# Kernel tuning notes

Hardware: AMD Instinct MI355X
Metric: run time of the kernel (lower is better)

Reference implementation:

```python
import jax, jax.numpy as jnp
from jax import lax
import numpy as np

B, CIN, COUT, T, H, W, KH, KW = 8, 256, 256, 16, 28, 28, 3, 3


def setup_inputs() -> dict:
    key = jax.random.key(0)
    k1, k2, k3 = jax.random.split(key, 3)
    x = jax.random.normal(k1, (B, CIN, T, H, W), dtype=jnp.float32)
    alpha = jax.random.uniform(k2, (B, CIN, T, 1, 1), dtype=jnp.float32)
    # base weight, kaiming-uniform-like init, stored as [1,1,c_out,c_in,kh,kw]
    fan_in = CIN * KH * KW
    bound = 1.0 / np.sqrt(fan_in)
    weight = jax.random.uniform(k3, (1, 1, COUT, CIN, KH, KW), dtype=jnp.float32,
                                minval=-bound, maxval=bound)
    return {"x": x, "alpha": alpha, "weight": weight}


def reference(x, alpha, weight):
    # x: [b, c_in, t, h, w]; alpha: [b, c_in, t, 1, 1]; weight: [1,1,c_out,c_in,kh,kw]
    b, c_in, t, h, w = x.shape
    c_out = weight.shape[2]
    w_base = weight[0, 0]  # [c_out, c_in, kh, kw]
    # W_t = alpha_t * W_base scales only input channels (alpha broadcasts over c_out),
    # so (alpha*W) conv x == W conv (alpha*x): modulate input, then one shared conv.
    xm = x * alpha  # [b, c_in, t, h, w]
    xm = jnp.transpose(xm, (0, 2, 1, 3, 4)).reshape(b * t, c_in, h, w)
    y = lax.conv_general_dilated(
        xm, w_base,
        window_strides=(1, 1),
        padding=((1, 1), (1, 1)),
        dimension_numbers=("NCHW", "OIHW", "NCHW"),
    )  # [b*t, c_out, h, w]
    oh, ow = y.shape[-2], y.shape[-1]
    y = y.reshape(b, t, c_out, oh, ow)
    return jnp.transpose(y, (0, 2, 1, 3, 4))  # [b, c_out, t, h, w]
```

## Files before the change

kernel.cpp:

```cpp
#include <hip/hip_runtime.h>
#include <hip/hip_bf16.h>
#include <cstdint>

#define CIN   256
#define COUT  256
#define NB    8
#define NT    16
#define NH    28
#define NW    28
#define HP    30
#define WP    30

#define XM_ELEMS   ((size_t)NB * NT * HP * WP * CIN)
#define XM_BYTES   (XM_ELEMS * 2)

typedef __bf16 bf16x8 __attribute__((ext_vector_type(8)));
typedef float  f32x4  __attribute__((ext_vector_type(4)));

#define AS1 __attribute__((address_space(1)))
#define AS3 __attribute__((address_space(3)))

static __device__ __forceinline__ unsigned short f2bf(float f) {
    __hip_bfloat16 h = __float2bfloat16(f);
    return __builtin_bit_cast(unsigned short, h);
}

__global__ void modulate_kernel(const float* __restrict__ x,
                                const float* __restrict__ alpha,
                                unsigned short* __restrict__ xm) {
    const int ci = threadIdx.x;
    const int blk = blockIdx.x;
    const int hp = blk % 30;
    const int bt = blk / 30;
    unsigned short* row = xm + (size_t)(bt * 900 + hp * 30) * 256;
    if (hp == 0 || hp == 29) {
        #pragma unroll
        for (int wp = 0; wp < 30; ++wp) row[wp * 256 + ci] = 0;
        return;
    }
    const int t = bt & 15, b = bt >> 4;
    const int h = hp - 1;
    const float a = alpha[(b * CIN + ci) * NT + t];
    const float* xrow = x + ((size_t)((b * CIN + ci) * NT + t) * NH + h) * NW;
    row[ci] = 0;
    row[29 * 256 + ci] = 0;
    const float4* xv = (const float4*)xrow;
    #pragma unroll
    for (int q = 0; q < 7; ++q) {
        float4 v = xv[q];
        row[(q * 4 + 1) * 256 + ci] = f2bf(v.x * a);
        row[(q * 4 + 2) * 256 + ci] = f2bf(v.y * a);
        row[(q * 4 + 3) * 256 + ci] = f2bf(v.z * a);
        row[(q * 4 + 4) * 256 + ci] = f2bf(v.w * a);
    }
}

__global__ void repack_w_kernel(const float* __restrict__ w,
                                unsigned short* __restrict__ wB) {
    const int ci = threadIdx.x;
    const int tap = blockIdx.x >> 8;
    const int co  = blockIdx.x & 255;
    wB[((tap * 256 + co) * 256) + ci] = f2bf(w[(co * 256 + ci) * 9 + tap]);
}


#define STAGE_A4(buf, off) do {                                               \
    _Pragma("unroll") for (int c_ = 0; c_ < 4; ++c_)                          \
        __builtin_amdgcn_global_load_lds(                                     \
            (const AS1 void*)(aSrc + (off) + c_ * 16384),                     \
            (AS3 void*)(lds + (buf)*32768 + c_*4096 + wave*512 + lane*8),     \
            16, 0, 0);                                                        \
} while (0)

#define STAGE_B4(buf, off) do {                                               \
    __builtin_amdgcn_global_load_lds((const AS1 void*)(bP0 + (off)),          \
        (AS3 void*)(lds + (buf)*32768 + 16384 + 0*4096 + wave*512 + lane*8), 16, 0, 0); \
    __builtin_amdgcn_global_load_lds((const AS1 void*)(bP1 + (off)),          \
        (AS3 void*)(lds + (buf)*32768 + 16384 + 1*4096 + wave*512 + lane*8), 16, 0, 0); \
    __builtin_amdgcn_global_load_lds((const AS1 void*)(bP2 + (off)),          \
        (AS3 void*)(lds + (buf)*32768 + 16384 + 2*4096 + wave*512 + lane*8), 16, 0, 0); \
    __builtin_amdgcn_global_load_lds((const AS1 void*)(bP3 + (off)),          \
        (AS3 void*)(lds + (buf)*32768 + 16384 + 3*4096 + wave*512 + lane*8), 16, 0, 0); \
} while (0)

#define READ_FA(buf) do {                                                     \
    _Pragma("unroll") for (int m_ = 0; m_ < 4; ++m_)                          \
    _Pragma("unroll") for (int kk_ = 0; kk_ < 2; ++kk_)                       \
        fa[m_][kk_] = *(const bf16x8*)(ldsc + (buf)*65536 +                   \
            (wm*64 + m_*16 + l15)*128 + (frag_sw ^ (kk_<<6)));                \
} while (0)

#define READ_FB4(buf, base) do {                                              \
    _Pragma("unroll") for (int f_ = 0; f_ < 4; ++f_)                          \
    _Pragma("unroll") for (int kk_ = 0; kk_ < 2; ++kk_)                       \
        fb[f_][kk_] = *(const bf16x8*)(ldsc + (buf)*65536 + 32768 +           \
            (wn*112 + ((base)+f_)*16 + l15)*128 + (frag_sw ^ (kk_<<6)));      \
} while (0)

#define READ_FB3(buf, base) do {                                              \
    _Pragma("unroll") for (int f_ = 0; f_ < 3; ++f_)                          \
    _Pragma("unroll") for (int kk_ = 0; kk_ < 2; ++kk_)                       \
        fb[f_][kk_] = *(const bf16x8*)(ldsc + (buf)*65536 + 32768 +           \
            (wn*112 + ((base)+f_)*16 + l15)*128 + (frag_sw ^ (kk_<<6)));      \
} while (0)

#define MFMA_A() do {                                                         \
    _Pragma("unroll") for (int m_ = 0; m_ < 4; ++m_)                          \
    _Pragma("unroll") for (int f_ = 0; f_ < 4; ++f_)                          \
    _Pragma("unroll") for (int kk_ = 0; kk_ < 2; ++kk_)                       \
        acc[m_][f_] = __builtin_amdgcn_mfma_f32_16x16x32_bf16(                \
            fb[f_][kk_], fa[m_][kk_], acc[m_][f_], 0, 0, 0);                  \
} while (0)

#define MFMA_B() do {                                                         \
    _Pragma("unroll") for (int m_ = 0; m_ < 4; ++m_)                          \
    _Pragma("unroll") for (int f_ = 0; f_ < 3; ++f_)                          \
    _Pragma("unroll") for (int kk_ = 0; kk_ < 2; ++kk_)                       \
        acc[m_][4+f_] = __builtin_amdgcn_mfma_f32_16x16x32_bf16(              \
            fb[f_][kk_], fa[m_][kk_], acc[m_][4+f_], 0, 0, 0);                \
} while (0)

#define BAR()   __builtin_amdgcn_s_barrier()
#define LGKM0() asm volatile("s_waitcnt lgkmcnt(0)")
#define VMW(N)  asm volatile("s_waitcnt vmcnt(" #N ")" ::: "memory")
#define PRIO(x) __builtin_amdgcn_s_setprio(x)

#define OFFA(kt) (((kt) >> 2) * 65536 + ((kt) & 3) * 64)
#define OFFB(kt) (((((kt) >> 2) / 3) - 1) * 7680 + ((((kt) >> 2) % 3) - 1) * 256 + ((kt) & 3) * 64)

__global__ __launch_bounds__(512, 2) void conv_gemm_kernel(
    const unsigned short* __restrict__ xm,
    const unsigned short* __restrict__ wB,
    float* __restrict__ out) {
    __shared__ unsigned short lds[65536];

    const int tid  = threadIdx.x;
    const int wave = tid >> 6;
    const int lane = tid & 63;
    const int n0   = blockIdx.x * 224;
    const int wm   = wave >> 1;
    const int wn   = wave & 1;
    const int l15  = lane & 15;

    const int swz8 = 8 * ((lane & 7) ^ (lane >> 3));
    const unsigned short* aSrc = wB + (wave * 8 + (lane >> 3)) * 256 + swz8;

    auto bcent = [&](int rowl) -> const unsigned short* {
        int r = rowl > 223 ? 223 : rowl;
        int n = n0 + r;
        int w_ = n % 28, h_ = (n / 28) % 28, bt = n / 784;
        return xm + (size_t)((bt * 30 + h_ + 1) * 30 + (w_ + 1)) * 256 + swz8;
    };
    const unsigned short* bP0 = bcent(0 * 64 + wave * 8 + (lane >> 3));
    const unsigned short* bP1 = bcent(1 * 64 + wave * 8 + (lane >> 3));
    const unsigned short* bP2 = bcent(2 * 64 + wave * 8 + (lane >> 3));
    const unsigned short* bP3 = bcent(3 * 64 + wave * 8 + (lane >> 3));

    const char* ldsc = (const char*)lds;
    const int frag_sw = ((lane >> 4) * 16) ^ ((lane & 7) << 4);

    f32x4 acc[4][7];
    #pragma unroll
    for (int i = 0; i < 4; ++i)
        #pragma unroll
        for (int j = 0; j < 7; ++j) acc[i][j] = f32x4{0.f,0.f,0.f,0.f};

    bf16x8 fa[4][2], fb[4][2];

    STAGE_A4(0, 0);
    STAGE_B4(0, OFFB(0));
    STAGE_A4(1, OFFA(1));
    VMW(4);
    BAR();

    #pragma unroll 1
    for (int it = 0; it < 17; ++it) {
        const int kt1 = 2 * it + 1;
        const int ka  = 2 * it + 2;
        const int kb  = 2 * it + 3;
        const int offB_k1 = OFFB(kt1);
        const int offA_ka = OFFA(ka);
        const int offB_ka = OFFB(ka);
        const int offA_kb = OFFA(kb);

        READ_FA(0); READ_FB4(0, 0);
        STAGE_B4(1, offB_k1);
        BAR(); LGKM0(); PRIO(1); MFMA_A(); PRIO(0); BAR();
        READ_FB3(0, 4);
        STAGE_A4(0, offA_ka);
        VMW(4);
        BAR(); LGKM0(); PRIO(1); MFMA_B(); PRIO(0); BAR();
        READ_FA(1); READ_FB4(1, 0);
        STAGE_B4(0, offB_ka);
        BAR(); LGKM0(); PRIO(1); MFMA_A(); PRIO(0); BAR();
        READ_FB3(1, 4);
        STAGE_A4(1, offA_kb);
        VMW(4);
        BAR(); LGKM0(); PRIO(1); MFMA_B(); PRIO(0); BAR();
    }

    {
        READ_FA(0); READ_FB4(0, 0);
        STAGE_B4(1, OFFB(35));
        BAR(); LGKM0(); PRIO(1); MFMA_A(); PRIO(0); BAR();
        READ_FB3(0, 4);
        VMW(0);
        BAR(); LGKM0(); PRIO(1); MFMA_B(); PRIO(0); BAR();
        READ_FA(1); READ_FB4(1, 0);
        LGKM0(); PRIO(1); MFMA_A(); PRIO(0);
        READ_FB3(1, 4);
        LGKM0(); PRIO(1); MFMA_B(); PRIO(0);
    }

    #pragma unroll
    for (int f = 0; f < 7; ++f) {
        const int n  = n0 + wn * 112 + f * 16 + ((lane >> 4) << 2);
        const int bt = n / 784;
        const int hw = n - bt * 784;
        const int b = bt >> 4, t = bt & 15;
        float* obase = out + ((size_t)(b * 256) * 16 + t) * 784 + hw;
        #pragma unroll
        for (int m = 0; m < 4; ++m) {
            const int co = wm * 64 + m * 16 + l15;
            *(f32x4*)(obase + (size_t)co * 12544) = acc[m][f];
        }
    }
}

extern "C" void kernel_launch(void* const* d_in, const int* in_sizes, int n_in,
                              void* d_out, int out_size, void* d_ws, size_t ws_size,
                              hipStream_t stream) {
    const float* x      = (const float*)d_in[0];
    const float* alpha  = (const float*)d_in[1];
    const float* weight = (const float*)d_in[2];
    float* out = (float*)d_out;

    unsigned short* xm = (unsigned short*)d_ws;
    unsigned short* wB = (unsigned short*)((char*)d_ws + XM_BYTES);

    modulate_kernel<<<dim3(NB * NT * HP), dim3(256), 0, stream>>>(x, alpha, xm);
    repack_w_kernel<<<dim3(9 * 256), dim3(256), 0, stream>>>(weight, wB);
    conv_gemm_kernel<<<dim3(448), dim3(512), 0, stream>>>(xm, wB, out);
}
```

Baseline: 162.5 us.

## Stage padded input halo once per channel block and reuse across taps

Result: slower. 313.1 us (+92.6%).

```diff
diff --git a/kernel.cpp b/kernel.cpp
--- a/kernel.cpp
+++ b/kernel.cpp
@@ -13,6 +13,7 @@
 
 #define XM_ELEMS   ((size_t)NB * NT * HP * WP * CIN)
 #define XM_BYTES   (XM_ELEMS * 2)
+#define SPAT_MAX   (NB * NT * HP * WP - 1)
 
 typedef __bf16 bf16x8 __attribute__((ext_vector_type(8)));
 typedef float  f32x4  __attribute__((ext_vector_type(4)));
@@ -64,44 +65,47 @@
 }
 
 
-#define STAGE_A4(buf, off) do {                                               \
+#define STAGE_A(abuf, offE) do {                                              \
     _Pragma("unroll") for (int c_ = 0; c_ < 4; ++c_)                          \
         __builtin_amdgcn_global_load_lds(                                     \
-            (const AS1 void*)(aSrc + (off) + c_ * 16384),                     \
-            (AS3 void*)(lds + (buf)*32768 + c_*4096 + wave*512 + lane*8),     \
+            (const AS1 void*)(aSrc + (offE) + c_ * 16384),                    \
+            (AS3 void*)(lds + (abuf)*16384 + c_*4096 + wave*512 + lane*8),    \
             16, 0, 0);                                                        \
 } while (0)
 
-#define STAGE_B4(buf, off) do {                                               \
-    __builtin_amdgcn_global_load_lds((const AS1 void*)(bP0 + (off)),          \
-        (AS3 void*)(lds + (buf)*32768 + 16384 + 0*4096 + wave*512 + lane*8), 16, 0, 0); \
-    __builtin_amdgcn_global_load_lds((const AS1 void*)(bP1 + (off)),          \
-        (AS3 void*)(lds + (buf)*32768 + 16384 + 1*4096 + wave*512 + lane*8), 16, 0, 0); \
-    __builtin_amdgcn_global_load_lds((const AS1 void*)(bP2 + (off)),          \
-        (AS3 void*)(lds + (buf)*32768 + 16384 + 2*4096 + wave*512 + lane*8), 16, 0, 0); \
-    __builtin_amdgcn_global_load_lds((const AS1 void*)(bP3 + (off)),          \
-        (AS3 void*)(lds + (buf)*32768 + 16384 + 3*4096 + wave*512 + lane*8), 16, 0, 0); \
-} while (0)
-
-#define READ_FA(buf) do {                                                     \
+#define STAGE_HALO(hbuf, ci0) do {                                            \
+    _Pragma("unroll") for (int c_ = 0; c_ < 5; ++c_) {                        \
+        int row_ = c_*64 + wave*8 + (lane>>3);                                \
+        int spat_ = haloSpat0 + row_;                                         \
+        spat_ = spat_ > SPAT_MAX ? SPAT_MAX : spat_;                          \
+        __builtin_amdgcn_global_load_lds(                                     \
+            (const AS1 void*)(xm + (size_t)spat_*256 + (ci0) + swz8),         \
+            (AS3 void*)(lds + 32768 + (hbuf)*23040 + (c_*64 + wave*8)*64 + lane*8), \
+            16, 0, 0);                                                        \
+    }                                                                         \
+    {   int rg_ = (wave < 5) ? (320 + wave*8) : ((wave - 5)*8);               \
+        int row_ = rg_ + (lane>>3);                                           \
+        int spat_ = haloSpat0 + row_;                                         \
+        spat_ = spat_ > SPAT_MAX ? SPAT_MAX : spat_;                          \
+        __builtin_amdgcn_global_load_lds(                                     \
+            (const AS1 void*)(xm + (size_t)spat_*256 + (ci0) + swz8),         \
+            (AS3 void*)(lds + 32768 + (hbuf)*23040 + rg_*64 + lane*8),        \
+            16, 0, 0); }                                                      \
+} while (0)
+
+#define READ_FA(abuf) do {                                                    \
     _Pragma("unroll") for (int m_ = 0; m_ < 4; ++m_)                          \
     _Pragma("unroll") for (int kk_ = 0; kk_ < 2; ++kk_)                       \
-        fa[m_][kk_] = *(const bf16x8*)(ldsc + (buf)*65536 +                   \
-            (wm*64 + m_*16 + l15)*128 + (frag_sw ^ (kk_<<6)));                \
-} while (0)
-
-#define READ_FB4(buf, base) do {                                              \
-    _Pragma("unroll") for (int f_ = 0; f_ < 4; ++f_)                          \
-    _Pragma("unroll") for (int kk_ = 0; kk_ < 2; ++kk_)                       \
-        fb[f_][kk_] = *(const bf16x8*)(ldsc + (buf)*65536 + 32768 +           \
-            (wn*112 + ((base)+f_)*16 + l15)*128 + (frag_sw ^ (kk_<<6)));      \
-} while (0)
-
-#define READ_FB3(buf, base) do {                                              \
-    _Pragma("unroll") for (int f_ = 0; f_ < 3; ++f_)                          \
-    _Pragma("unroll") for (int kk_ = 0; kk_ < 2; ++kk_)                       \
-        fb[f_][kk_] = *(const bf16x8*)(ldsc + (buf)*65536 + 32768 +           \
-            (wn*112 + ((base)+f_)*16 + l15)*128 + (frag_sw ^ (kk_<<6)));      \
+        fa[m_][kk_] = *(const bf16x8*)(lds + (abuf)*16384 +                   \
+            (wm*64 + m_*16 + l15)*64 + (kslot ^ (kk_*32)));                   \
+} while (0)
+
+#define READ_FB1(slot, hbuf, f_, TO) do {                                     \
+    const int row_ = localB[f_] + (TO);                                       \
+    const int sw_  = ((lane>>4)*8) ^ ((row_ & 7)*8);                          \
+    _Pragma("unroll") for (int kk_ = 0; kk_ < 2; ++kk_)                       \
+        fb[slot][kk_] = *(const bf16x8*)(lds + 32768 + (hbuf)*23040 +         \
+            row_*64 + (sw_ ^ (kk_*32)));                                      \
 } while (0)
 
 #define MFMA_A() do {                                                         \
@@ -121,18 +125,14 @@
 } while (0)
 
 #define BAR()   __builtin_amdgcn_s_barrier()
-#define LGKM0() asm volatile("s_waitcnt lgkmcnt(0)")
 #define VMW(N)  asm volatile("s_waitcnt vmcnt(" #N ")" ::: "memory")
 #define PRIO(x) __builtin_amdgcn_s_setprio(x)
-
-#define OFFA(kt) (((kt) >> 2) * 65536 + ((kt) & 3) * 64)
-#define OFFB(kt) (((((kt) >> 2) / 3) - 1) * 7680 + ((((kt) >> 2) % 3) - 1) * 256 + ((kt) & 3) * 64)
 
 __global__ __launch_bounds__(512, 2) void conv_gemm_kernel(
     const unsigned short* __restrict__ xm,
     const unsigned short* __restrict__ wB,
     float* __restrict__ out) {
-    __shared__ unsigned short lds[65536];
+    __shared__ unsigned short lds[78848];
 
     const int tid  = threadIdx.x;
     const int wave = tid >> 6;
@@ -141,24 +141,25 @@
     const int wm   = wave >> 1;
     const int wn   = wave & 1;
     const int l15  = lane & 15;
-
-    const int swz8 = 8 * ((lane & 7) ^ (lane >> 3));
+    const int kslot = ((lane >> 4) * 8) ^ ((l15 & 7) * 8);
+
+    const int r0 = blockIdx.x * 8;
+    const int prow_start = r0 + 2 * (r0 / 28);
+    const int haloSpat0  = prow_start * 30;
+
+    int localB[7];
+    #pragma unroll
+    for (int f = 0; f < 7; ++f) {
+        const int m = wn * 112 + f * 16 + l15;
+        const int r = r0 + m / 28;
+        const int w_ = m % 28;
+        const int prow_c = r + 2 * (r / 28) + 1;
+        localB[f] = (prow_c - prow_start) * 30 + (w_ + 1);
+    }
+
+    const int swz8 = 8 * ((lane & 7) ^ ((lane >> 3) & 7));
     const unsigned short* aSrc = wB + (wave * 8 + (lane >> 3)) * 256 + swz8;
 
-    auto bcent = [&](int rowl) -> const unsigned short* {
-        int r = rowl > 223 ? 223 : rowl;
-        int n = n0 + r;
-        int w_ = n % 28, h_ = (n / 28) % 28, bt = n / 784;
-        return xm + (size_t)((bt * 30 + h_ + 1) * 30 + (w_ + 1)) * 256 + swz8;
-    };
-    const unsigned short* bP0 = bcent(0 * 64 + wave * 8 + (lane >> 3));
-    const unsigned short* bP1 = bcent(1 * 64 + wave * 8 + (lane >> 3));
-    const unsigned short* bP2 = bcent(2 * 64 + wave * 8 + (lane >> 3));
-    const unsigned short* bP3 = bcent(3 * 64 + wave * 8 + (lane >> 3));
-
-    const char* ldsc = (const char*)lds;
-    const int frag_sw = ((lane >> 4) * 16) ^ ((lane & 7) << 4);
-
     f32x4 acc[4][7];
     #pragma unroll
     for (int i = 0; i < 4; ++i)
@@ -167,49 +168,46 @@
 
     bf16x8 fa[4][2], fb[4][2];
 
-    STAGE_A4(0, 0);
-    STAGE_B4(0, OFFB(0));
-    STAGE_A4(1, OFFA(1));
-    VMW(4);
+
+    STAGE_A(0, 0);
+    STAGE_HALO(0, 0);
+    VMW(0);
     BAR();
 
     #pragma unroll 1
-    for (int it = 0; it < 17; ++it) {
-        const int kt1 = 2 * it + 1;
-        const int ka  = 2 * it + 2;
-        const int kb  = 2 * it + 3;
-        const int offB_k1 = OFFB(kt1);
-        const int offA_ka = OFFA(ka);
-        const int offB_ka = OFFB(ka);
-        const int offA_kb = OFFA(kb);
-
-        READ_FA(0); READ_FB4(0, 0);
-        STAGE_B4(1, offB_k1);
-        BAR(); LGKM0(); PRIO(1); MFMA_A(); PRIO(0); BAR();
-        READ_FB3(0, 4);
-        STAGE_A4(0, offA_ka);
-        VMW(4);
-        BAR(); LGKM0(); PRIO(1); MFMA_B(); PRIO(0); BAR();
-        READ_FA(1); READ_FB4(1, 0);
-        STAGE_B4(0, offB_ka);
-        BAR(); LGKM0(); PRIO(1); MFMA_A(); PRIO(0); BAR();
-        READ_FB3(1, 4);
-        STAGE_A4(1, offA_kb);
-        VMW(4);
-        BAR(); LGKM0(); PRIO(1); MFMA_B(); PRIO(0); BAR();
-    }
-
-    {
-        READ_FA(0); READ_FB4(0, 0);
-        STAGE_B4(1, OFFB(35));
-        BAR(); LGKM0(); PRIO(1); MFMA_A(); PRIO(0); BAR();
-        READ_FB3(0, 4);
-        VMW(0);
-        BAR(); LGKM0(); PRIO(1); MFMA_B(); PRIO(0); BAR();
-        READ_FA(1); READ_FB4(1, 0);
-        LGKM0(); PRIO(1); MFMA_A(); PRIO(0);
-        READ_FB3(1, 4);
-        LGKM0(); PRIO(1); MFMA_B(); PRIO(0);
+    for (int cb = 0; cb < 4; ++cb) {
+        const int hb = cb & 1;
+        #pragma unroll
+        for (int tap = 0; tap < 9; ++tap) {
+            const int kt = cb * 9 + tap;
+            const int ab = kt & 1;
+            const int TO = ((tap / 3) - 1) * 30 + ((tap % 3) - 1);
+
+            READ_FA(ab);
+            READ_FB1(0, hb, 0, TO);
+            READ_FB1(1, hb, 1, TO);
+            READ_FB1(2, hb, 2, TO);
+            READ_FB1(3, hb, 3, TO);
+
+            if (!(cb == 3 && tap == 8)) {
+                const int tapN = (tap == 8) ? 0 : tap + 1;
+                const int cbN  = (tap == 8) ? cb + 1 : cb;
+                STAGE_A(ab ^ 1, tapN * 65536 + cbN * 64);
+            }
+            if (tap == 6 && cb < 3) STAGE_HALO(hb ^ 1, (cb + 1) * 64);
+
+            PRIO(1);
+            MFMA_A();
+            READ_FB1(0, hb, 4, TO);
+            READ_FB1(1, hb, 5, TO);
+            READ_FB1(2, hb, 6, TO);
+            MFMA_B();
+            PRIO(0);
+
+            if (tap == 6 && cb < 3) { VMW(6); }
+            else                    { VMW(0); }
+            BAR();
+        }
     }
 
     #pragma unroll
```
